# Performance work log

Hardware: AMD Instinct MI355X
Metric: run time of the kernel (lower is better)

Reference implementation:

```python
import jax, jax.numpy as jnp
import numpy as np

B, N, D_IN, D_OUT, NHOP = 16, 1024, 128, 128, 3


def setup_inputs() -> dict:
    key = jax.random.key(0)
    ks = jax.random.split(key, 7)
    x = jax.random.normal(ks[0], (B, N, D_IN), dtype=jnp.float32)
    # sparse-ish binary adjacency (float, as in the torch model) with self loops
    adj = (jax.random.uniform(ks[1], (B, N, N)) < 0.05).astype(jnp.float32)
    adj = jnp.maximum(adj, jnp.eye(N, dtype=jnp.float32)[None])
    # learned params (torch nn.Linear default-ish init scale)
    s_in = 1.0 / np.sqrt(D_IN)
    s_out = 1.0 / np.sqrt(2 * D_OUT)
    W_w = jax.random.uniform(ks[2], (D_OUT, D_IN), minval=-s_in, maxval=s_in, dtype=jnp.float32)
    W_b = jax.random.uniform(ks[3], (D_OUT,), minval=-s_in, maxval=s_in, dtype=jnp.float32)
    A = jax.random.normal(ks[4], (D_OUT, D_OUT), dtype=jnp.float32) * 0.02  # nn.Parameter(zeros) would kill signal; use small init
    gate_w = jax.random.uniform(ks[5], (1, 2 * D_OUT), minval=-s_out, maxval=s_out, dtype=jnp.float32)
    gate_b = jax.random.uniform(ks[6], (1,), minval=-s_out, maxval=s_out, dtype=jnp.float32)
    return {"x": x, "adj": adj, "W_w": W_w, "W_b": W_b, "A": A,
            "gate_w": gate_w, "gate_b": gate_b}


def reference(x, adj, W_w, W_b, A, gate_w, gate_b):
    # h = W(x): [B,N,D_OUT]
    h = jnp.einsum('bnd,od->bno', x, W_w) + W_b
    # bilinear score e[b,j,k] = (h A)_j . h_k, symmetrized
    e = jnp.einsum('bjl,bkl->bjk', jnp.einsum('bjd,de->bje', h, A), h)
    e = e + jnp.swapaxes(e, 1, 2)
    # masked softmax over dim=1 (as in the torch code), then re-mask
    att = jnp.where(adj > 0, e, jnp.zeros((), dtype=e.dtype))
    att = jax.nn.softmax(att, axis=1)
    att = att * adj
    retval = h
    for _ in range(NHOP):
        az = jax.nn.relu(jnp.einsum('bij,bjk->bik', att, retval))
        gate_in = jnp.concatenate([h, az], axis=-1)            # [B,N,2*D_OUT]
        coeff = jax.nn.sigmoid(jnp.einsum('bnf,of->bno', gate_in, gate_w) + gate_b)  # [B,N,1]
        retval = coeff * h + (1.0 - coeff) * az
    return retval
```

## Files before the change

kernel.cpp:

```cpp
#include <hip/hip_runtime.h>
#include <math.h>

#define Bn 16
#define Nn 1024
#define Dn 128

typedef unsigned short ushort;
typedef unsigned long long u64;
typedef short short8 __attribute__((ext_vector_type(8)));
typedef float f32x4 __attribute__((ext_vector_type(4)));
typedef ushort us8 __attribute__((ext_vector_type(8)));
typedef ushort us4 __attribute__((ext_vector_type(4)));

__device__ __forceinline__ ushort f2bf(float f) {
    unsigned u = __float_as_uint(f);
    u += 0x7fff + ((u >> 16) & 1);
    return (ushort)(u >> 16);
}
__device__ __forceinline__ float bf2f(ushort s) {
    return __uint_as_float(((unsigned)s) << 16);
}

#if defined(__has_builtin)
#if __has_builtin(__builtin_amdgcn_global_load_lds)
#define HAVE_GLL 1
#endif
#endif
#ifndef HAVE_GLL
#define HAVE_GLL 0
#endif

typedef __attribute__((address_space(1))) void as1_t;
typedef __attribute__((address_space(3))) void as3_t;

__device__ __forceinline__ void stage_group(const void* gbase, void* lbase, int lane) {
#if HAVE_GLL
    __builtin_amdgcn_global_load_lds((as1_t*)((const char*)gbase + lane * 16),
                                     (as3_t*)lbase, 16, 0, 0);
#else
    *(us8*)((char*)lbase + lane * 16) = *(const us8*)((const char*)gbase + lane * 16);
#endif
}


__global__ __launch_bounds__(256) void k_ph0(const float* __restrict__ Ww,
                                             const float* __restrict__ A,
                                             const float* __restrict__ adj,
                                             ushort* __restrict__ Whi, ushort* __restrict__ Wlo,
                                             ushort* __restrict__ AThi, ushort* __restrict__ ATlo,
                                             float* __restrict__ Z, u64* __restrict__ bm) {
    int L = blockIdx.x, t = threadIdx.x;
    if (L < 64) {
        int i = L * 256 + t;
        float w = Ww[i];
        ushort wh = f2bf(w);
        Whi[i] = wh;
        Wlo[i] = f2bf(w - bf2f(wh));
        int e = i >> 7, d = i & 127;
        float a = A[d * Dn + e];
        ushort ah = f2bf(a);
        AThi[i] = ah;
        ATlo[i] = f2bf(a - bf2f(ah));
        Z[i] = (float)Nn;
    }
    int gwv = L * 4 + (t >> 6);
    int lane = t & 63;
    #pragma unroll 4
    for (int it = 0; it < 16; ++it) {
        int pair = gwv * 16 + it;
        const float* p = adj + (size_t)pair * 256 + lane * 4;
        float4 v = *(const float4*)p;
        u64 b0 = __ballot(v.x > 0.f);
        u64 b1 = __ballot(v.y > 0.f);
        u64 b2 = __ballot(v.z > 0.f);
        u64 b3 = __ballot(v.w > 0.f);
        if (lane == 0) {
            u64* d = bm + (size_t)pair * 4;
            d[0] = b0; d[1] = b1; d[2] = b2; d[3] = b3;
        }
    }
}

__global__ __launch_bounds__(256) void k_h(const float* __restrict__ x,
                                           const float* __restrict__ Wb,
                                           const ushort* __restrict__ Whi,
                                           const ushort* __restrict__ Wlo,
                                           const ushort* __restrict__ AThi,
                                           const ushort* __restrict__ ATlo,
                                           float* __restrict__ h,
                                           ushort* __restrict__ h16f,
                                           ushort* __restrict__ hA16f) {
    int I0 = blockIdx.x * 16;
    int t = threadIdx.x, w = t >> 6, lane = t & 63;
    int m = lane & 15, q = lane >> 4;

    __shared__ float xs[16][Dn + 4];
    __shared__ float hs[16][Dn + 4];
    __shared__ float has[16][Dn + 4];

    {
        int r = t >> 4, c8 = (t & 15) * 8;
        const float* src = x + (size_t)(I0 + r) * Dn + c8;
        *(float4*)&xs[r][c8]     = *(const float4*)(src);
        *(float4*)&xs[r][c8 + 4] = *(const float4*)(src + 4);
    }
    __syncthreads();

    f32x4 acc0 = {0,0,0,0}, acc1 = {0,0,0,0};
    #pragma unroll
    for (int ks = 0; ks < 4; ++ks) {
        int k0 = q * 8 + ks * 32;
        float v[8]; short8 ahi, alo;
        *(float4*)(v)     = *(const float4*)(&xs[m][k0]);
        *(float4*)(v + 4) = *(const float4*)(&xs[m][k0 + 4]);
        #pragma unroll
        for (int j = 0; j < 8; ++j) {
            ushort hi = f2bf(v[j]);
            ahi[j] = (short)hi;
            alo[j] = (short)f2bf(v[j] - bf2f(hi));
        }
        #pragma unroll
        for (int nn = 0; nn < 2; ++nn) {
            int brow = (w * 2 + nn) * 16 + m;
            short8 bhi = __builtin_bit_cast(short8, ((const us8*)(Whi + (size_t)brow * Dn))[q + ks * 4]);
            short8 blo = __builtin_bit_cast(short8, ((const us8*)(Wlo + (size_t)brow * Dn))[q + ks * 4]);
            f32x4 acc = nn ? acc1 : acc0;
            acc = __builtin_amdgcn_mfma_f32_16x16x32_bf16(ahi, bhi, acc, 0, 0, 0);
            acc = __builtin_amdgcn_mfma_f32_16x16x32_bf16(alo, bhi, acc, 0, 0, 0);
            acc = __builtin_amdgcn_mfma_f32_16x16x32_bf16(ahi, blo, acc, 0, 0, 0);
            if (nn) acc1 = acc; else acc0 = acc;
        }
    }
    #pragma unroll
    for (int nn = 0; nn < 2; ++nn) {
        int col = (w * 2 + nn) * 16 + m;
        float bias = Wb[col];
        f32x4 acc = nn ? acc1 : acc0;
        #pragma unroll
        for (int r = 0; r < 4; ++r) {
            int rl = q * 4 + r;
            float hv = acc[r] + bias;
            h[(size_t)(I0 + rl) * Dn + col] = hv;
            hs[rl][col] = hv;
        }
    }
    __syncthreads();

    f32x4 bcc0 = {0,0,0,0}, bcc1 = {0,0,0,0};
    #pragma unroll
    for (int ks = 0; ks < 4; ++ks) {
        int k0 = q * 8 + ks * 32;
        float v[8]; short8 ahi, alo;
        *(float4*)(v)     = *(const float4*)(&hs[m][k0]);
        *(float4*)(v + 4) = *(const float4*)(&hs[m][k0 + 4]);
        #pragma unroll
        for (int j = 0; j < 8; ++j) {
            ushort hi = f2bf(v[j]);
            ahi[j] = (short)hi;
            alo[j] = (short)f2bf(v[j] - bf2f(hi));
        }
        #pragma unroll
        for (int nn = 0; nn < 2; ++nn) {
            int brow = (w * 2 + nn) * 16 + m;
            short8 bhi = __builtin_bit_cast(short8, ((const us8*)(AThi + (size_t)brow * Dn))[q + ks * 4]);
            short8 blo = __builtin_bit_cast(short8, ((const us8*)(ATlo + (size_t)brow * Dn))[q + ks * 4]);
            f32x4 acc = nn ? bcc1 : bcc0;
            acc = __builtin_amdgcn_mfma_f32_16x16x32_bf16(ahi, bhi, acc, 0, 0, 0);
            acc = __builtin_amdgcn_mfma_f32_16x16x32_bf16(alo, bhi, acc, 0, 0, 0);
            acc = __builtin_amdgcn_mfma_f32_16x16x32_bf16(ahi, blo, acc, 0, 0, 0);
            if (nn) bcc1 = acc; else bcc0 = acc;
        }
    }
    #pragma unroll
    for (int nn = 0; nn < 2; ++nn) {
        int col = (w * 2 + nn) * 16 + m;
        f32x4 acc = nn ? bcc1 : bcc0;
        #pragma unroll
        for (int r = 0; r < 4; ++r)
            has[q * 4 + r][col] = acc[r];
    }
    __syncthreads();

    {
        int kc = t >> 6, mm = (t >> 2) & 15, qq = t & 3;
        int cb = kc * 32 + qq * 8;
        us8 oh, oa;
        #pragma unroll
        for (int e = 0; e < 8; ++e) {
            oh[e] = f2bf(hs[mm][cb + e]);
            oa[e] = f2bf(has[mm][cb + e]);
        }
        size_t U = (size_t)(I0 >> 4) * 256 + kc * 64 + mm * 4 + qq;
        ((us8*)h16f)[U]  = oh;
        ((us8*)hA16f)[U] = oa;
    }
}

__global__ __launch_bounds__(256, 2) void k_scores(const ushort* __restrict__ h16f,
                                                   const ushort* __restrict__ hA16f,
                                                   const u64* __restrict__ bm,
                                                   ushort* __restrict__ Ef,
                                                   float* __restrict__ Z) {
    int L = blockIdx.x;
    int b    = ((L & 7) << 1) | (L >> 11);
    int tile = (L >> 3) & 255;
    int I0 = (tile >> 4) << 6;
    int J0 = (tile & 15) << 6;
    int t = threadIdx.x, wid = t >> 6, lane = t & 63;
    int m = lane & 15, q = lane >> 4;

    __shared__ __align__(16) char smem[66560];
    float (*sc)[68] = (float(*)[68])smem;
    float (*cz)[64] = (float(*)[64])(smem + 65536);

    {
        const char* hb  = (const char*)h16f  + (size_t)b * 16384 * 16;
        const char* ab  = (const char*)hA16f + (size_t)b * 16384 * 16;
        for (int g = wid; g < 64; g += 4) {
            int arr = g >> 4, rt_l = (g >> 2) & 3, kk = g & 3;
            int rbase = ((arr < 2) ? (I0 >> 4) : (J0 >> 4)) + rt_l;
            const char* base = (arr & 1) ? ab : hb;
            const char* gp = base + ((size_t)rbase * 256 + kk * 64) * 16;
            stage_group(gp, smem + g * 1024, lane);
        }
    }
    __syncthreads();

    int off16 = (m * 4 + q) * 16;
    f32x4 acc[4] = {};
    #pragma unroll
    for (int ks = 0; ks < 4; ++ks) {
        short8 a1 = __builtin_bit_cast(short8, *(const us8*)(smem + 16384 + (wid * 4 + ks) * 1024 + off16));
        short8 a2 = __builtin_bit_cast(short8, *(const us8*)(smem +         (wid * 4 + ks) * 1024 + off16));
        #pragma unroll
        for (int nt = 0; nt < 4; ++nt) {
            short8 b1 = __builtin_bit_cast(short8, *(const us8*)(smem + 32768 + (nt * 4 + ks) * 1024 + off16));
            short8 b2 = __builtin_bit_cast(short8, *(const us8*)(smem + 49152 + (nt * 4 + ks) * 1024 + off16));
            acc[nt] = __builtin_amdgcn_mfma_f32_16x16x32_bf16(a1, b1, acc[nt], 0, 0, 0);
            acc[nt] = __builtin_amdgcn_mfma_f32_16x16x32_bf16(a2, b2, acc[nt], 0, 0, 0);
        }
    }
    __syncthreads();

    #pragma unroll
    for (int nt = 0; nt < 4; ++nt)
        #pragma unroll
        for (int r = 0; r < 4; ++r)
            sc[wid * 16 + q * 4 + r][nt * 16 + m] = acc[nt][r];
    __syncthreads();

    int row16 = t >> 4, c = t & 15;
    int bitc = ((J0 >> 2) & 63) + c;
    float colsum[4] = {0.f, 0.f, 0.f, 0.f};
    #pragma unroll
    for (int it = 0; it < 4; ++it) {
        int row = it * 16 + row16;
        const u64* wp = bm + ((size_t)(b * Nn + I0 + row) * 4 + (J0 >> 8)) * 4;
        u64 wj[4] = {wp[0], wp[1], wp[2], wp[3]};
        float s4[4];
        *(float4*)s4 = *(const float4*)(&sc[row][c * 4]);
        us4 e4;
        #pragma unroll
        for (int j = 0; j < 4; ++j) {
            float ex = __expf(s4[j]);
            bool on = (wj[j] >> bitc) & 1;
            e4[j] = f2bf(on ? ex : 0.f);
            colsum[j] += on ? (ex - 1.0f) : 0.f;
        }
        size_t U = ((((size_t)b * 64 + (I0 >> 4) + it) * 32 + (J0 >> 5) + (c >> 3)) * 16 + row16) * 4
                 + ((c & 7) >> 1);
        *(us4*)(Ef + U * 8 + (c & 1) * 4) = e4;
    }
    #pragma unroll
    for (int j = 0; j < 4; ++j) {
        colsum[j] += __shfl_xor(colsum[j], 16, 64);
        colsum[j] += __shfl_xor(colsum[j], 32, 64);
    }
    if (lane < 16) {
        #pragma unroll
        for (int j = 0; j < 4; ++j) cz[wid][lane * 4 + j] = colsum[j];
    }
    __syncthreads();
    if (t < 64) {
        float s = cz[0][t] + cz[1][t] + cz[2][t] + cz[3][t];
        atomicAdd(&Z[b * Nn + J0 + t], s);
    }
}

__global__ __launch_bounds__(256) void k_prep(const float* __restrict__ src,
                                              const float* __restrict__ Z,
                                              ushort* __restrict__ Tf) {
    int b = blockIdx.y;
    int j0 = blockIdx.x * 64;
    int t = threadIdx.x;
    __shared__ float ls[64][129];
    __shared__ float iz[64];
    if (t < 64) iz[t] = 1.0f / Z[b * Nn + j0 + t];
    __syncthreads();
    #pragma unroll
    for (int it = 0; it < 8; ++it) {
        int idx = it * 256 + t;
        int j = idx >> 5, k4 = (idx & 31) * 4;
        float4 v = *(const float4*)(src + ((size_t)b * Nn + j0 + j) * Dn + k4);
        float z = iz[j];
        ls[j][k4] = v.x * z; ls[j][k4 + 1] = v.y * z;
        ls[j][k4 + 2] = v.z * z; ls[j][k4 + 3] = v.w * z;
    }
    __syncthreads();
    int k = t & 127, half = t >> 7;
    us8 o[4];
    #pragma unroll
    for (int qq = 0; qq < 4; ++qq) {
        us8 tmp;
        #pragma unroll
        for (int e = 0; e < 8; ++e)
            tmp[e] = f2bf(ls[half * 32 + qq * 8 + e][k]);
        o[qq] = tmp;
    }
    size_t U = (((size_t)(k >> 4) * 32 + (j0 >> 5) + half) * 16 + (k & 15)) * 4;
    us8* dst = (us8*)(Tf + (size_t)b * 131072 + U * 8);
    dst[0] = o[0]; dst[1] = o[1]; dst[2] = o[2]; dst[3] = o[3];
}

__global__ __launch_bounds__(256) void k_hop(const ushort* __restrict__ Ef,
                                             const ushort* __restrict__ Tf,
                                             const float* __restrict__ h,
                                             const float* __restrict__ Z,
                                             const float* __restrict__ gw,
                                             const float* __restrict__ gb,
                                             ushort* __restrict__ Tfn,
                                             float* __restrict__ out,
                                             int last) {
    int L = blockIdx.x;
    int b  = ((L & 7) << 1) | (L >> 7);
    int t4 = (L >> 3) & 15;
    int t = threadIdx.x, w = t >> 6, lane = t & 63;
    int m = lane & 15, q = lane >> 4;
    int rt = t4 * 4 + w;
    int I0 = rt << 4;

    __shared__ __align__(16) char smem[49152];
    int off16 = (m * 4 + q) * 16;

    f32x4 acc[8] = {};
    for (int cch = 0; cch < 8; ++cch) {
        for (int g = w; g < 48; g += 4) {
            const char* gp; char* lp;
            if (g < 16) {
                int rr = g >> 2, kk = g & 3;
                gp = (const char*)Ef + ((((size_t)b * 64 + t4 * 4 + rr) * 32 + cch * 4 + kk) * 64) * 16;
                lp = smem + g * 1024;
            } else {
                int gb2 = g - 16, nt = gb2 >> 2, kk = gb2 & 3;
                gp = (const char*)Tf + ((((size_t)b * 8 + nt) * 32 + cch * 4 + kk) * 64) * 16;
                lp = smem + 16384 + gb2 * 1024;
            }
            stage_group(gp, lp, lane);
        }
        __syncthreads();

        #pragma unroll
        for (int kk = 0; kk < 4; ++kk) {
            short8 a = __builtin_bit_cast(short8, *(const us8*)(smem + (w * 4 + kk) * 1024 + off16));
            #pragma unroll
            for (int nt = 0; nt < 8; ++nt) {
                short8 bf = __builtin_bit_cast(short8,
                    *(const us8*)(smem + 16384 + (nt * 4 + kk) * 1024 + off16));
                acc[nt] = __builtin_amdgcn_mfma_f32_16x16x32_bf16(a, bf, acc[nt], 0, 0, 0);
            }
        }
        __syncthreads();
    }

    float gb0 = gb[0];
    float gwa[8], gwz[8];
    #pragma unroll
    for (int nt = 0; nt < 8; ++nt) { gwa[nt] = gw[nt * 16 + m]; gwz[nt] = gw[Dn + nt * 16 + m]; }

    float hv[8][4], coef[4];
    size_t hbase = ((size_t)b * Nn + I0) * Dn;
    #pragma unroll
    for (int r = 0; r < 4; ++r) {
        int row = q * 4 + r;
        float gs = 0.f;
        #pragma unroll
        for (int nt = 0; nt < 8; ++nt) {
            float az = fmaxf(acc[nt][r], 0.f);
            acc[nt][r] = az;
            float hh = h[hbase + (size_t)row * Dn + nt * 16 + m];
            hv[nt][r] = hh;
            gs += hh * gwa[nt] + az * gwz[nt];
        }
        gs += __shfl_xor(gs, 1, 64);
        gs += __shfl_xor(gs, 2, 64);
        gs += __shfl_xor(gs, 4, 64);
        gs += __shfl_xor(gs, 8, 64);
        coef[r] = 1.0f / (1.0f + __expf(-(gs + gb0)));
    }

    if (last) {
        #pragma unroll
        for (int r = 0; r < 4; ++r) {
            int row = q * 4 + r;
            float cc = coef[r];
            #pragma unroll
            for (int nt = 0; nt < 8; ++nt)
                out[hbase + (size_t)row * Dn + nt * 16 + m] =
                    cc * hv[nt][r] + (1.f - cc) * acc[nt][r];
        }
    } else {
        ushort (*tt)[128][16] = (ushort(*)[128][16])smem;
        #pragma unroll
        for (int r = 0; r < 4; ++r) {
            int row = q * 4 + r;
            float cc = coef[r];
            float iz = 1.0f / Z[b * Nn + I0 + row];
            #pragma unroll
            for (int nt = 0; nt < 8; ++nt) {
                float v = cc * hv[nt][r] + (1.f - cc) * acc[nt][r];
                tt[w][nt * 16 + m][row] = f2bf(v * iz);
            }
        }
        __syncthreads();
        int k = t >> 1, jh = t & 1;
        size_t U0 = (((size_t)(k >> 4) * 32 + t4 * 2 + jh) * 16 + (k & 15)) * 4;
        ushort* dst = Tfn + (size_t)b * 131072 + U0 * 8;
        #pragma unroll
        for (int qq = 0; qq < 4; ++qq)
            *(us8*)(dst + qq * 8) = *(const us8*)&tt[jh * 2 + (qq >> 1)][k][(qq & 1) * 8];
    }
}

extern "C" void kernel_launch(void* const* d_in, const int* in_sizes, int n_in,
                              void* d_out, int out_size, void* d_ws, size_t ws_size,
                              hipStream_t stream) {
    const float* x    = (const float*)d_in[0];
    const float* adj  = (const float*)d_in[1];
    const float* Ww   = (const float*)d_in[2];
    const float* Wb   = (const float*)d_in[3];
    const float* A    = (const float*)d_in[4];
    const float* gw   = (const float*)d_in[5];
    const float* gb   = (const float*)d_in[6];
    float* out = (float*)d_out;

    char* ws = (char*)d_ws;
    float*  h    = (float*)(ws);
    ushort* Ta   = (ushort*)(ws + (8u << 20));
    ushort* Tb   = (ushort*)(ws + (12u << 20));
    ushort* E    = (ushort*)(ws + (16u << 20));
    float*  Z    = (float*)(ws + (48u << 20));
    ushort* Whi  = (ushort*)(ws + (48u << 20) + (64u << 10));
    ushort* Wlo  = (ushort*)(ws + (48u << 20) + (96u << 10));
    ushort* AThi = (ushort*)(ws + (48u << 20) + (128u << 10));
    ushort* ATlo = (ushort*)(ws + (48u << 20) + (160u << 10));
    u64*    bm   = (u64*)(ws + (48u << 20) + (192u << 10));

    k_ph0   <<<1024, 256, 0, stream>>>(Ww, A, adj, Whi, Wlo, AThi, ATlo, Z, bm);
    k_h     <<<1024, 256, 0, stream>>>(x, Wb, Whi, Wlo, AThi, ATlo, h, Ta, Tb);
    k_scores<<<4096, 256, 0, stream>>>(Ta, Tb, bm, E, Z);
    k_prep  <<<dim3(16, Bn), 256, 0, stream>>>(h, Z, Ta);
    k_hop   <<<256, 256, 0, stream>>>(E, Ta, h, Z, gw, gb, Tb, out, 0);
    k_hop   <<<256, 256, 0, stream>>>(E, Tb, h, Z, gw, gb, Ta, out, 0);
    k_hop   <<<256, 256, 0, stream>>>(E, Ta, h, Z, gw, gb, (ushort*)nullptr, out, 1);
}
```

Measured before the change: 230.4 us.

## Fold symmetric score into single GEMM via A+A^T and double-buffer hop staging

The symmetrised bilinear score e+e^T is computed as h(A+A^T)h^T, so A+A^T is formed once in the prep kernel and the score kernel runs one MFMA chain instead of two. That halves its LDS staging, which shrinks shared memory and allows higher occupancy (launch bounds raised to 4). The hop kernel now loads the E fragments straight from global into registers and double-buffers the T tiles in LDS, prefetching the next chunk while computing the current one, with the chunk loop fully unrolled. The cost is different bf16 rounding of the summed matrix and more registers in k_hop, which now asks for only one block per CU.

```diff
diff --git a/kernel.cpp b/kernel.cpp
--- a/kernel.cpp
+++ b/kernel.cpp
@@ -47,7 +47,7 @@
                                              const float* __restrict__ A,
                                              const float* __restrict__ adj,
                                              ushort* __restrict__ Whi, ushort* __restrict__ Wlo,
-                                             ushort* __restrict__ AThi, ushort* __restrict__ ATlo,
+                                             ushort* __restrict__ Shi, ushort* __restrict__ Slo,
                                              float* __restrict__ Z, u64* __restrict__ bm) {
     int L = blockIdx.x, t = threadIdx.x;
     if (L < 64) {
@@ -57,10 +57,10 @@
         Whi[i] = wh;
         Wlo[i] = f2bf(w - bf2f(wh));
         int e = i >> 7, d = i & 127;
-        float a = A[d * Dn + e];
-        ushort ah = f2bf(a);
-        AThi[i] = ah;
-        ATlo[i] = f2bf(a - bf2f(ah));
+        float s = A[i] + A[d * Dn + e];
+        ushort sh = f2bf(s);
+        Shi[i] = sh;
+        Slo[i] = f2bf(s - bf2f(sh));
         Z[i] = (float)Nn;
     }
     int gwv = L * 4 + (t >> 6);
@@ -85,18 +85,18 @@
                                            const float* __restrict__ Wb,
                                            const ushort* __restrict__ Whi,
                                            const ushort* __restrict__ Wlo,
-                                           const ushort* __restrict__ AThi,
-                                           const ushort* __restrict__ ATlo,
+                                           const ushort* __restrict__ Shi,
+                                           const ushort* __restrict__ Slo,
                                            float* __restrict__ h,
                                            ushort* __restrict__ h16f,
-                                           ushort* __restrict__ hA16f) {
+                                           ushort* __restrict__ g16f) {
     int I0 = blockIdx.x * 16;
     int t = threadIdx.x, w = t >> 6, lane = t & 63;
     int m = lane & 15, q = lane >> 4;
 
     __shared__ float xs[16][Dn + 4];
     __shared__ float hs[16][Dn + 4];
-    __shared__ float has[16][Dn + 4];
+    __shared__ float gs_[16][Dn + 4];
 
     {
         int r = t >> 4, c8 = (t & 15) * 8;
@@ -162,8 +162,8 @@
         #pragma unroll
         for (int nn = 0; nn < 2; ++nn) {
             int brow = (w * 2 + nn) * 16 + m;
-            short8 bhi = __builtin_bit_cast(short8, ((const us8*)(AThi + (size_t)brow * Dn))[q + ks * 4]);
-            short8 blo = __builtin_bit_cast(short8, ((const us8*)(ATlo + (size_t)brow * Dn))[q + ks * 4]);
+            short8 bhi = __builtin_bit_cast(short8, ((const us8*)(Shi + (size_t)brow * Dn))[q + ks * 4]);
+            short8 blo = __builtin_bit_cast(short8, ((const us8*)(Slo + (size_t)brow * Dn))[q + ks * 4]);
             f32x4 acc = nn ? bcc1 : bcc0;
             acc = __builtin_amdgcn_mfma_f32_16x16x32_bf16(ahi, bhi, acc, 0, 0, 0);
             acc = __builtin_amdgcn_mfma_f32_16x16x32_bf16(alo, bhi, acc, 0, 0, 0);
@@ -177,7 +177,7 @@
         f32x4 acc = nn ? bcc1 : bcc0;
         #pragma unroll
         for (int r = 0; r < 4; ++r)
-            has[q * 4 + r][col] = acc[r];
+            gs_[q * 4 + r][col] = acc[r];
     }
     __syncthreads();
 
@@ -188,16 +188,16 @@
         #pragma unroll
         for (int e = 0; e < 8; ++e) {
             oh[e] = f2bf(hs[mm][cb + e]);
-            oa[e] = f2bf(has[mm][cb + e]);
+            oa[e] = f2bf(gs_[mm][cb + e]);
         }
         size_t U = (size_t)(I0 >> 4) * 256 + kc * 64 + mm * 4 + qq;
-        ((us8*)h16f)[U]  = oh;
-        ((us8*)hA16f)[U] = oa;
-    }
-}
-
-__global__ __launch_bounds__(256, 2) void k_scores(const ushort* __restrict__ h16f,
-                                                   const ushort* __restrict__ hA16f,
+        ((us8*)h16f)[U] = oh;
+        ((us8*)g16f)[U] = oa;
+    }
+}
+
+__global__ __launch_bounds__(256, 4) void k_scores(const ushort* __restrict__ g16f,
+                                                   const ushort* __restrict__ h16f,
                                                    const u64* __restrict__ bm,
                                                    ushort* __restrict__ Ef,
                                                    float* __restrict__ Z) {
@@ -208,36 +208,38 @@
     int J0 = (tile & 15) << 6;
     int t = threadIdx.x, wid = t >> 6, lane = t & 63;
     int m = lane & 15, q = lane >> 4;
-
-    __shared__ __align__(16) char smem[66560];
+    int off16 = (m * 4 + q) * 16;
+
+    __shared__ __align__(16) char smem[18432];
     float (*sc)[68] = (float(*)[68])smem;
-    float (*cz)[64] = (float(*)[64])(smem + 65536);
+    float (*cz)[64] = (float(*)[64])(smem + 17408);
 
     {
-        const char* hb  = (const char*)h16f  + (size_t)b * 16384 * 16;
-        const char* ab  = (const char*)hA16f + (size_t)b * 16384 * 16;
-        for (int g = wid; g < 64; g += 4) {
-            int arr = g >> 4, rt_l = (g >> 2) & 3, kk = g & 3;
-            int rbase = ((arr < 2) ? (I0 >> 4) : (J0 >> 4)) + rt_l;
-            const char* base = (arr & 1) ? ab : hb;
-            const char* gp = base + ((size_t)rbase * 256 + kk * 64) * 16;
-            stage_group(gp, smem + g * 1024, lane);
-        }
-    }
-    __syncthreads();
-
-    int off16 = (m * 4 + q) * 16;
+        const char* hbp = (const char*)h16f + (size_t)b * 262144;
+        for (int g = wid; g < 16; g += 4) {
+            int rt_l = g >> 2, kk = g & 3;
+            stage_group(hbp + ((size_t)((J0 >> 4) + rt_l) * 256 + kk * 64) * 16,
+                        smem + g * 1024, lane);
+        }
+    }
+    short8 afr[4];
+    {
+        const char* gbp = (const char*)g16f + (size_t)b * 262144
+                        + (size_t)((I0 >> 4) + wid) * 4096 + off16;
+        #pragma unroll
+        for (int ks = 0; ks < 4; ++ks)
+            afr[ks] = __builtin_bit_cast(short8, *(const us8*)(gbp + ks * 1024));
+    }
+    __syncthreads();
+
     f32x4 acc[4] = {};
     #pragma unroll
     for (int ks = 0; ks < 4; ++ks) {
-        short8 a1 = __builtin_bit_cast(short8, *(const us8*)(smem + 16384 + (wid * 4 + ks) * 1024 + off16));
-        short8 a2 = __builtin_bit_cast(short8, *(const us8*)(smem +         (wid * 4 + ks) * 1024 + off16));
         #pragma unroll
         for (int nt = 0; nt < 4; ++nt) {
-            short8 b1 = __builtin_bit_cast(short8, *(const us8*)(smem + 32768 + (nt * 4 + ks) * 1024 + off16));
-            short8 b2 = __builtin_bit_cast(short8, *(const us8*)(smem + 49152 + (nt * 4 + ks) * 1024 + off16));
-            acc[nt] = __builtin_amdgcn_mfma_f32_16x16x32_bf16(a1, b1, acc[nt], 0, 0, 0);
-            acc[nt] = __builtin_amdgcn_mfma_f32_16x16x32_bf16(a2, b2, acc[nt], 0, 0, 0);
+            short8 bb = __builtin_bit_cast(short8,
+                *(const us8*)(smem + (nt * 4 + ks) * 1024 + off16));
+            acc[nt] = __builtin_amdgcn_mfma_f32_16x16x32_bf16(afr[ks], bb, acc[nt], 0, 0, 0);
         }
     }
     __syncthreads();
@@ -322,15 +324,40 @@
     dst[0] = o[0]; dst[1] = o[1]; dst[2] = o[2]; dst[3] = o[3];
 }
 
-__global__ __launch_bounds__(256) void k_hop(const ushort* __restrict__ Ef,
-                                             const ushort* __restrict__ Tf,
-                                             const float* __restrict__ h,
-                                             const float* __restrict__ Z,
-                                             const float* __restrict__ gw,
-                                             const float* __restrict__ gb,
-                                             ushort* __restrict__ Tfn,
-                                             float* __restrict__ out,
-                                             int last) {
+#define STAGEB(buf, cch) do {                                                          \
+    for (int g = w; g < 32; g += 4) {                                                  \
+        stage_group(tfb + ((size_t)(g >> 2) * 32 + (cch) * 4 + (g & 3)) * 1024,        \
+                    smem + (buf) * 32768 + g * 1024, lane);                            \
+    } } while (0)
+
+#define HOP_CHUNK(cch, CUR, NXT)                                                       \
+    if ((cch) < 7) {                                                                   \
+        STAGEB(((cch) + 1) & 1, (cch) + 1);                                            \
+        _Pragma("unroll")                                                              \
+        for (int kk = 0; kk < 4; ++kk)                                                 \
+            NXT[kk] = __builtin_bit_cast(short8,                                       \
+                *(const us8*)(ebase + (((cch) + 1) * 4 + kk) * 1024));                 \
+    }                                                                                  \
+    _Pragma("unroll")                                                                  \
+    for (int kk = 0; kk < 4; ++kk) {                                                   \
+        _Pragma("unroll")                                                              \
+        for (int nt = 0; nt < 8; ++nt) {                                               \
+            short8 bf = __builtin_bit_cast(short8,                                     \
+                *(const us8*)(smem + ((cch) & 1) * 32768 + (nt * 4 + kk) * 1024 + off16)); \
+            acc[nt] = __builtin_amdgcn_mfma_f32_16x16x32_bf16(CUR[kk], bf, acc[nt], 0, 0, 0); \
+        }                                                                              \
+    }                                                                                  \
+    __syncthreads();
+
+__global__ __launch_bounds__(256, 1) void k_hop(const ushort* __restrict__ Ef,
+                                                const ushort* __restrict__ Tf,
+                                                const float* __restrict__ h,
+                                                const float* __restrict__ Z,
+                                                const float* __restrict__ gw,
+                                                const float* __restrict__ gb,
+                                                ushort* __restrict__ Tfn,
+                                                float* __restrict__ out,
+                                                int last) {
     int L = blockIdx.x;
     int b  = ((L & 7) << 1) | (L >> 7);
     int t4 = (L >> 3) & 15;
@@ -339,38 +366,29 @@
     int rt = t4 * 4 + w;
     int I0 = rt << 4;
 
-    __shared__ __align__(16) char smem[49152];
+    __shared__ __align__(16) char smem[65536];
     int off16 = (m * 4 + q) * 16;
 
+    const char* tfb   = (const char*)Tf + (size_t)b * 262144;
+    const char* ebase = (const char*)Ef + (size_t)(b * 64 + rt) * 32768 + off16;
+
     f32x4 acc[8] = {};
-    for (int cch = 0; cch < 8; ++cch) {
-        for (int g = w; g < 48; g += 4) {
-            const char* gp; char* lp;
-            if (g < 16) {
-                int rr = g >> 2, kk = g & 3;
-                gp = (const char*)Ef + ((((size_t)b * 64 + t4 * 4 + rr) * 32 + cch * 4 + kk) * 64) * 16;
-                lp = smem + g * 1024;
-            } else {
-                int gb2 = g - 16, nt = gb2 >> 2, kk = gb2 & 3;
-                gp = (const char*)Tf + ((((size_t)b * 8 + nt) * 32 + cch * 4 + kk) * 64) * 16;
-                lp = smem + 16384 + gb2 * 1024;
-            }
-            stage_group(gp, lp, lane);
-        }
-        __syncthreads();
-
-        #pragma unroll
-        for (int kk = 0; kk < 4; ++kk) {
-            short8 a = __builtin_bit_cast(short8, *(const us8*)(smem + (w * 4 + kk) * 1024 + off16));
-            #pragma unroll
-            for (int nt = 0; nt < 8; ++nt) {
-                short8 bf = __builtin_bit_cast(short8,
-                    *(const us8*)(smem + 16384 + (nt * 4 + kk) * 1024 + off16));
-                acc[nt] = __builtin_amdgcn_mfma_f32_16x16x32_bf16(a, bf, acc[nt], 0, 0, 0);
-            }
-        }
-        __syncthreads();
-    }
+    short8 aA[4], aB[4];
+
+    STAGEB(0, 0);
+    #pragma unroll
+    for (int kk = 0; kk < 4; ++kk)
+        aA[kk] = __builtin_bit_cast(short8, *(const us8*)(ebase + kk * 1024));
+    __syncthreads();
+
+    HOP_CHUNK(0, aA, aB)
+    HOP_CHUNK(1, aB, aA)
+    HOP_CHUNK(2, aA, aB)
+    HOP_CHUNK(3, aB, aA)
+    HOP_CHUNK(4, aA, aB)
+    HOP_CHUNK(5, aB, aA)
+    HOP_CHUNK(6, aA, aB)
+    HOP_CHUNK(7, aB, aA)
 
     float gb0 = gb[0];
     float gwa[8], gwz[8];
@@ -451,13 +469,13 @@
     float*  Z    = (float*)(ws + (48u << 20));
     ushort* Whi  = (ushort*)(ws + (48u << 20) + (64u << 10));
     ushort* Wlo  = (ushort*)(ws + (48u << 20) + (96u << 10));
-    ushort* AThi = (ushort*)(ws + (48u << 20) + (128u << 10));
-    ushort* ATlo = (ushort*)(ws + (48u << 20) + (160u << 10));
+    ushort* Shi  = (ushort*)(ws + (48u << 20) + (128u << 10));
+    ushort* Slo  = (ushort*)(ws + (48u << 20) + (160u << 10));
     u64*    bm   = (u64*)(ws + (48u << 20) + (192u << 10));
 
-    k_ph0   <<<1024, 256, 0, stream>>>(Ww, A, adj, Whi, Wlo, AThi, ATlo, Z, bm);
-    k_h     <<<1024, 256, 0, stream>>>(x, Wb, Whi, Wlo, AThi, ATlo, h, Ta, Tb);
-    k_scores<<<4096, 256, 0, stream>>>(Ta, Tb, bm, E, Z);
+    k_ph0   <<<1024, 256, 0, stream>>>(Ww, A, adj, Whi, Wlo, Shi, Slo, Z, bm);
+    k_h     <<<1024, 256, 0, stream>>>(x, Wb, Whi, Wlo, Shi, Slo, h, Ta, Tb);
+    k_scores<<<4096, 256, 0, stream>>>(Tb, Ta, bm, E, Z);
     k_prep  <<<dim3(16, Bn), 256, 0, stream>>>(h, Z, Ta);
     k_hop   <<<256, 256, 0, stream>>>(E, Ta, h, Z, gw, gb, Tb, out, 0);
     k_hop   <<<256, 256, 0, stream>>>(E, Tb, h, Z, gw, gb, Ta, out, 0);
```

Result: faster. 198.2 us (-13.9%).
